# Optimization experiments

Hardware: AMD Instinct MI355X
Metric: run time of the kernel (lower is better)

## Reference

```python
import jax, jax.numpy as jnp
import numpy as np

N = 50000          # nodes
E = 1_600_000      # directed edges (avg degree 32)
C_IN = 512
C_OUT = 64
H1, F1 = 8, 8      # conv1: heads=8, out per head=8
H2 = 1             # conv2: heads_2=1, concat=False
NEG_SLOPE = 0.2    # GATConv default leaky_relu slope
ELU_ALPHA = 0.2    # F.elu(..., alpha=0.2) in forward


def _glorot(key, shape):
    fan_in, fan_out = shape[0], shape[-1]
    lim = jnp.sqrt(6.0 / (fan_in + fan_out))
    return jax.random.uniform(key, shape, jnp.float32, -lim, lim)


def setup_inputs() -> dict:
    key = jax.random.key(0)
    ks = jax.random.split(key, 12)
    x = jax.random.normal(ks[0], (N, C_IN), jnp.float32)
    edge_index = jax.random.randint(ks[1], (2, E), 0, N, jnp.int32)
    # conv1 params
    W1 = _glorot(ks[2], (C_IN, H1 * F1))
    att_src1 = _glorot(ks[3], (H1, F1))
    att_dst1 = _glorot(ks[4], (H1, F1))
    b1 = jnp.zeros((H1 * F1,), jnp.float32)
    # conv2 params (concat=False, heads=1)
    W2 = _glorot(ks[5], (H1 * F1, H2 * C_OUT))
    att_src2 = _glorot(ks[6], (H2, C_OUT))
    att_dst2 = _glorot(ks[7], (H2, C_OUT))
    b2 = jnp.zeros((C_OUT,), jnp.float32)
    return dict(x=x, edge_index=edge_index, W1=W1, att_src1=att_src1,
                att_dst1=att_dst1, b1=b1, W2=W2, att_src2=att_src2,
                att_dst2=att_dst2, b2=b2)


def gat_conv(x, src, dst, W, att_src, att_dst, bias, concat):
    """PyG GATConv (self-loops already appended to src/dst). Eval mode (no dropout)."""
    n = x.shape[0]
    H, F = att_src.shape
    h = (x @ W).reshape(n, H, F)                       # [N,H,F]
    a_src = jnp.sum(h * att_src, axis=-1)              # [N,H]
    a_dst = jnp.sum(h * att_dst, axis=-1)              # [N,H]
    e = jax.nn.leaky_relu(a_src[src] + a_dst[dst], NEG_SLOPE)  # [E',H]
    # segment softmax over incoming edges of each destination node
    m = jax.ops.segment_max(e, dst, num_segments=n)    # [N,H]
    m = jnp.where(jnp.isfinite(m), m, 0.0)
    ex = jnp.exp(e - m[dst])
    denom = jax.ops.segment_sum(ex, dst, num_segments=n)
    alpha = ex / (denom[dst] + 1e-16)                  # [E',H]
    msg = h[src] * alpha[:, :, None]                   # [E',H,F]
    out = jax.ops.segment_sum(msg, dst, num_segments=n)  # [N,H,F]
    out = out.reshape(n, H * F) if concat else out.mean(axis=1)
    return out + bias


def reference(x, edge_index, W1, att_src1, att_dst1, b1,
              W2, att_src2, att_dst2, b2):
    # add self loops once (GATConv default add_self_loops=True)
    loop = jnp.arange(N, dtype=edge_index.dtype)
    src = jnp.concatenate([edge_index[0], loop])
    dst = jnp.concatenate([edge_index[1], loop])
    # dropout layers are identity in eval mode
    h = gat_conv(x, src, dst, W1, att_src1, att_dst1, b1, concat=True)
    h = jax.nn.elu(h, alpha=ELU_ALPHA)
    out = gat_conv(h, src, dst, W2, att_src2, att_dst2, b2, concat=False)
    return out
```

## Files before the change

### kernel.cpp

```cpp
#include <hip/hip_runtime.h>
#include <hip/hip_bf16.h>
#include <hip/hip_fp16.h>

constexpr int NN   = 50000;
constexpr int NE   = 1600000;
constexpr int CIN  = 512;
constexpr int DH   = 64;
constexpr int H1N  = 8;

constexpr int NB     = 98;
constexpr int TILE   = 8192;
constexpr int NTILES = (NE + TILE - 1) / TILE;
constexpr int BCAP   = 20480;

typedef __attribute__((ext_vector_type(8))) short bf16x8v;
typedef __attribute__((ext_vector_type(4))) float f32x4v;

__device__ __forceinline__ float bf(unsigned short u) {
    union { unsigned int i; float f; } v; v.i = ((unsigned int)u) << 16; return v.f;
}
__device__ __forceinline__ float lrelu(float x) { return fmaxf(x, 0.2f * x); }
__device__ __forceinline__ float ldf(const unsigned short* p, size_t i, bool f32) {
    return f32 ? ((const float*)p)[i] : bf(p[i]);
}
__device__ __forceinline__ unsigned short f2bf(float f) {
    union { float f; unsigned int u; } v; v.f = f;
    unsigned int r = (v.u + 0x7fff + ((v.u >> 16) & 1)) >> 16;
    return (unsigned short)r;
}

__global__ __launch_bounds__(256) void gat_detect(const unsigned short* __restrict__ W1,
                                                  int* __restrict__ flag) {
    __shared__ int cnt;
    if (threadIdx.x == 0) cnt = 0;
    __syncthreads();
    int local = 0;
    for (int i = threadIdx.x; i < 4096; i += 256) {
        unsigned short u = W1[i];
        int e = (u >> 7) & 0xFF;
        if (e >= 140) local++;
    }
    atomicAdd(&cnt, local);
    __syncthreads();
    if (threadIdx.x == 0) flag[0] = (cnt > 100) ? 1 : 0;
}


__global__ __launch_bounds__(256) void gat_bucketA(const int* __restrict__ src,
                                                   const int* __restrict__ dst,
                                                   int* __restrict__ gcnt,
                                                   unsigned int* __restrict__ bucketed) {
    __shared__ int hist[NB];
    __shared__ int cur[NB];
    int t = threadIdx.x;
    if (t < NB) hist[t] = 0;
    __syncthreads();
    int base = blockIdx.x * TILE;
    for (int i = t; i < TILE; i += 256) {
        int e = base + i;
        if (e < NE) atomicAdd(&hist[dst[e] >> 9], 1);
    }
    __syncthreads();
    if (t < NB) cur[t] = hist[t] ? atomicAdd(&gcnt[t], hist[t]) : 0;
    __syncthreads();
    for (int i = t; i < TILE; i += 256) {
        int e = base + i;
        if (e < NE) {
            int d = dst[e];
            int b = d >> 9;
            int p = atomicAdd(&cur[b], 1);
            if (p < BCAP)
                bucketed[(size_t)b * BCAP + p] =
                    ((unsigned int)(d & 511) << 16) | (unsigned int)src[e];
        }
    }
}

__global__ __launch_bounds__(128) void gat_bucketscan(const int* __restrict__ gcnt,
                                                      int* __restrict__ boff,
                                                      int* __restrict__ row_ptr) {
    __shared__ int s[128];
    int t = threadIdx.x;
    s[t] = (t < NB) ? gcnt[t] : 0;
    __syncthreads();
    for (int off = 1; off < 128; off <<= 1) {
        int x = s[t];
        int add = (t >= off) ? s[t - off] : 0;
        __syncthreads();
        s[t] = x + add;
        __syncthreads();
    }
    if (t <= NB) boff[t] = (t == 0) ? 0 : s[t - 1];
    if (t == 0) row_ptr[NN] = NE;
}

__global__ __launch_bounds__(256) void gat_bucketB(const unsigned int* __restrict__ bucketed,
                                                   const int* __restrict__ gcnt,
                                                   const int* __restrict__ boff,
                                                   int* __restrict__ row_ptr,
                                                   int* __restrict__ col_idx) {
    __shared__ int hist[512];
    __shared__ int sums[256];
    int t = threadIdx.x;
    int b = blockIdx.x;
    int e0 = boff[b];
    int cnt = gcnt[b]; if (cnt > BCAP) cnt = BCAP;
    const unsigned int* bb = bucketed + (size_t)b * BCAP;
    hist[t] = 0; hist[t + 256] = 0;
    __syncthreads();
    for (int i = t; i < cnt; i += 256)
        atomicAdd(&hist[bb[i] >> 16], 1);
    __syncthreads();
    int a0 = hist[2 * t], a1 = hist[2 * t + 1];
    sums[t] = a0 + a1;
    __syncthreads();
    for (int off = 1; off < 256; off <<= 1) {
        int x = sums[t];
        int add = (t >= off) ? sums[t - off] : 0;
        __syncthreads();
        sums[t] = x + add;
        __syncthreads();
    }
    int excl = (t == 0) ? 0 : sums[t - 1];
    hist[2 * t]     = excl;
    hist[2 * t + 1] = excl + a0;
    int node0 = b << 9;
    if (node0 + 2 * t     < NN) row_ptr[node0 + 2 * t]     = e0 + excl;
    if (node0 + 2 * t + 1 < NN) row_ptr[node0 + 2 * t + 1] = e0 + excl + a0;
    __syncthreads();
    for (int i = t; i < cnt; i += 256) {
        unsigned int pk = bb[i];
        int p = atomicAdd(&hist[pk >> 16], 1);
        col_idx[e0 + p] = (int)(pk & 0xFFFFu);
    }
}


__global__ __launch_bounds__(256) void gat_maxcol(const float* __restrict__ v, int n, int H,
                                                  unsigned int* __restrict__ out) {
    __shared__ float red[256];
    int t = threadIdx.x;
    float mx = -3.4e38f;
    for (int idx = blockIdx.x * 256 + t; idx < n; idx += gridDim.x * 256)
        mx = fmaxf(mx, v[idx]);
    red[t] = mx;
    __syncthreads();
    for (int off = 128; off >= H; off >>= 1) {
        if (t < off) red[t] = fmaxf(red[t], red[t + off]);
        __syncthreads();
    }
    if (t < H) {
        union { float f; unsigned int u; } b; b.f = red[t];
        unsigned int enc = (b.u & 0x80000000u) ? ~b.u : (b.u | 0x80000000u);
        atomicMax(&out[t], enc);
    }
}

__device__ __forceinline__ float gdecode(unsigned int u) {
    union { unsigned int u; float f; } d;
    d.u = (u & 0x80000000u) ? (u ^ 0x80000000u) : ~u;
    return d.f;
}


__global__ __launch_bounds__(256) void gat_transW(const unsigned short* __restrict__ W1,
                                                  const int* __restrict__ flag,
                                                  unsigned short* __restrict__ wts) {
    int idx = blockIdx.x * 256 + threadIdx.x;
    int n = idx >> 9, k = idx & 511;
    if (flag[0] == 0) {
        int o  = n * 1024 + k * 2;
        int os = o ^ ((n & 7) << 4);
        wts[os >> 1] = W1[(size_t)k * DH + n];
    } else {
        float v = ((const float*)W1)[(size_t)k * DH + n];
        unsigned short hi = f2bf(v);
        union { unsigned int u; float f; } hf; hf.u = ((unsigned int)hi) << 16;
        unsigned short lo = f2bf(v - hf.f);
        int q = k >> 7, kk = k & 127;
        int o = q * 32768 + n * 256 + ((kk * 2) ^ ((n & 7) << 4));
        wts[o >> 1]             = hi;
        wts[(o + 16384) >> 1]   = lo;
    }
}


__global__ __launch_bounds__(256) void gat_transW2(const unsigned short* __restrict__ W2,
                                                   const int* __restrict__ flag,
                                                   unsigned short* __restrict__ wts2) {
    int idx = blockIdx.x * 256 + threadIdx.x;
    if (idx >= 4096) return;
    int n = idx & 63, k = idx >> 6;
    unsigned short hi, lo;
    if (flag[0] == 0) {
        hi = W2[(size_t)k * DH + n];
        lo = 0;
    } else {
        float v = ((const float*)W2)[(size_t)k * DH + n];
        hi = f2bf(v);
        union { unsigned int u; float f; } hf; hf.u = ((unsigned int)hi) << 16;
        lo = f2bf(v - hf.f);
    }
    int o = n * 128 + ((k * 2) ^ ((n & 7) << 4));
    wts2[o >> 1]            = hi;
    wts2[(o + 8192) >> 1]   = lo;
}


__global__ __launch_bounds__(256) void gat_gemm1_mfma(const unsigned short* __restrict__ x,
                                                      const unsigned short* __restrict__ wts,
                                                      const unsigned short* __restrict__ as1,
                                                      const unsigned short* __restrict__ ad1,
                                                      const int* __restrict__ flag,
                                                      __half* __restrict__ h1h,
                                                      float* __restrict__ a_s1,
                                                      float* __restrict__ a_d1) {
    if (flag[0] != 0) return;
    __shared__ __align__(16) unsigned short wl[32768];
    int t = threadIdx.x;
#pragma unroll
    for (int it = 0; it < 16; ++it) {
        int c = it * 256 + t;
        *(uint4*)((char*)wl + c * 16) = *(const uint4*)((const char*)wts + c * 16);
    }
    __syncthreads();

    int lane = t & 63, wv = t >> 6;
    int g = lane >> 4;
    int r = lane & 15;
    int chunk = blockIdx.x * 4 + wv;
    if (chunk * 16 >= NN) return;
    int rowbase = chunk * 16;

    int vbase = r * 1024;
    int gx = g * 16;
    int xr = (r & 7) << 4;

    const char* xrow = (const char*)x + ((size_t)(rowbase + r) * CIN + g * 8) * 2;

    f32x4v acc[4];
#pragma unroll
    for (int nt = 0; nt < 4; ++nt) acc[nt] = (f32x4v){0.f, 0.f, 0.f, 0.f};

#pragma unroll 4
    for (int s = 0; s < 16; ++s) {
        union { uint4 u; bf16x8v v; } a;
        a.u = *(const uint4*)(xrow + s * 64);
        int o = vbase + ((s * 64 + gx) ^ xr);
        const char* bp = (const char*)wl + o;
#pragma unroll
        for (int nt = 0; nt < 4; ++nt) {
            union { uint4 u; bf16x8v v; } bv;
            bv.u = *(const uint4*)(bp + nt * 16384);
            acc[nt] = __builtin_amdgcn_mfma_f32_16x16x32_bf16(a.v, bv.v, acc[nt], 0, 0, 0);
        }
    }

    float avs[4], avd[4];
#pragma unroll
    for (int nt = 0; nt < 4; ++nt) {
        avs[nt] = bf(as1[nt * 16 + r]);
        avd[nt] = bf(ad1[nt * 16 + r]);
    }

#pragma unroll
    for (int nt = 0; nt < 4; ++nt) {
#pragma unroll
        for (int i = 0; i < 4; ++i) {
            int row = rowbase + g * 4 + i;
            float v = acc[nt][i];
            h1h[(size_t)row * DH + nt * 16 + r] = __float2half(v);
            float ps = v * avs[nt];
            float pd = v * avd[nt];
            ps += __shfl_xor(ps, 1, 64); ps += __shfl_xor(ps, 2, 64); ps += __shfl_xor(ps, 4, 64);
            pd += __shfl_xor(pd, 1, 64); pd += __shfl_xor(pd, 2, 64); pd += __shfl_xor(pd, 4, 64);
            if ((r & 7) == 0) {
                int head = nt * 2 + (r >> 3);
                a_s1[row * H1N + head] = ps;
                a_d1[row * H1N + head] = pd;
            }
        }
    }
}


__global__ __launch_bounds__(256) void gat_gemm1_mfma_f32(const float* __restrict__ x,
                                                          const unsigned short* __restrict__ wts,
                                                          const float* __restrict__ as1,
                                                          const float* __restrict__ ad1,
                                                          const int* __restrict__ flag,
                                                          __half* __restrict__ h1h,
                                                          float* __restrict__ a_s1,
                                                          float* __restrict__ a_d1) {
    if (flag[0] == 0) return;
    __shared__ __align__(16) unsigned short wl[16384];
    int t = threadIdx.x;
    int lane = t & 63, wv = t >> 6;
    int g = lane >> 4;
    int r = lane & 15;
    int chunk = blockIdx.x * 4 + wv;
    bool active = (chunk * 16 < NN);
    int rowbase = (active ? chunk : 0) * 16;

    int vbase = r * 256;
    int xr = (r & 7) << 4;

    const float* xrow = x + (size_t)(rowbase + r) * CIN + g * 8;

    f32x4v acc[4];
#pragma unroll
    for (int nt = 0; nt < 4; ++nt) acc[nt] = (f32x4v){0.f, 0.f, 0.f, 0.f};

    for (int q = 0; q < 4; ++q) {
        if (q) __syncthreads();
        const uint4* gsrc = (const uint4*)((const char*)wts + q * 32768);
#pragma unroll
        for (int it = 0; it < 8; ++it)
            ((uint4*)wl)[it * 256 + t] = gsrc[it * 256 + t];
        __syncthreads();

#pragma unroll
        for (int s = 0; s < 4; ++s) {
            const float4* xp = (const float4*)(xrow + q * 128 + s * 32);
            float4 v0 = xp[0], v1 = xp[1];
            float xv[8] = {v0.x, v0.y, v0.z, v0.w, v1.x, v1.y, v1.z, v1.w};
            union { unsigned short u[8]; bf16x8v v; } ahi, alo;
#pragma unroll
            for (int i2 = 0; i2 < 8; ++i2) {
                union { float f; unsigned int u; } xb; xb.f = xv[i2];
                unsigned int hb = xb.u & 0xffff0000u;
                union { unsigned int u; float f; } hf; hf.u = hb;
                ahi.u[i2] = (unsigned short)(xb.u >> 16);
                alo.u[i2] = f2bf(xv[i2] - hf.f);
            }
            int o = vbase + ((s * 64 + g * 16) ^ xr);
#pragma unroll
            for (int nt = 0; nt < 4; ++nt) {
                union { uint4 u; bf16x8v v; } bhi, blo;
                bhi.u = *(const uint4*)((const char*)wl + nt * 4096 + o);
                blo.u = *(const uint4*)((const char*)wl + 16384 + nt * 4096 + o);
                acc[nt] = __builtin_amdgcn_mfma_f32_16x16x32_bf16(ahi.v, bhi.v, acc[nt], 0, 0, 0);
                acc[nt] = __builtin_amdgcn_mfma_f32_16x16x32_bf16(ahi.v, blo.v, acc[nt], 0, 0, 0);
                acc[nt] = __builtin_amdgcn_mfma_f32_16x16x32_bf16(alo.v, bhi.v, acc[nt], 0, 0, 0);
            }
        }
    }

    if (!active) return;

    float avs[4], avd[4];
#pragma unroll
    for (int nt = 0; nt < 4; ++nt) {
        avs[nt] = as1[nt * 16 + r];
        avd[nt] = ad1[nt * 16 + r];
    }

#pragma unroll
    for (int nt = 0; nt < 4; ++nt) {
#pragma unroll
        for (int i = 0; i < 4; ++i) {
            int row = rowbase + g * 4 + i;
            float v = acc[nt][i];
            h1h[(size_t)row * DH + nt * 16 + r] = __float2half(v);
            float ps = v * avs[nt];
            float pd = v * avd[nt];
            ps += __shfl_xor(ps, 1, 64); ps += __shfl_xor(ps, 2, 64); ps += __shfl_xor(ps, 4, 64);
            pd += __shfl_xor(pd, 1, 64); pd += __shfl_xor(pd, 2, 64); pd += __shfl_xor(pd, 4, 64);
            if ((r & 7) == 0) {
                int head = nt * 2 + (r >> 3);
                a_s1[row * H1N + head] = ps;
                a_d1[row * H1N + head] = pd;
            }
        }
    }
}


__global__ __launch_bounds__(256) void gat_agg1(const int* __restrict__ row_ptr,
                                                const int* __restrict__ col_idx,
                                                const float* __restrict__ a_s1,
                                                const float* __restrict__ a_d1,
                                                const unsigned int* __restrict__ Gsu,
                                                const __half* __restrict__ h1h,
                                                const unsigned short* __restrict__ b1,
                                                const int* __restrict__ flag,
                                                float* __restrict__ hout) {
    const bool f32 = (flag[0] != 0);
    int i = (blockIdx.x * 256 + threadIdx.x) >> 6;
    int lane = threadIdx.x & 63;
    if (i >= NN) return;
    int ek = lane & 7;
    int eh = lane >> 3;
    int wbase = lane & ~7;

    float adst = a_d1[i * H1N + eh];
    float m = lrelu(gdecode(Gsu[eh]) + adst);

    int jb = row_ptr[i], je = row_ptr[i + 1];
    int deg = je - jb;
    int myidx = (lane < deg) ? col_idx[jb + lane] : 0;

    float wself = __expf(lrelu(a_s1[i * H1N + eh] + adst) - m);
    float denp = (ek == 0) ? wself : 0.f;
    float acc = wself * __half2float(h1h[(size_t)i * DH + lane]);

    for (int j0 = 0; j0 < deg; j0 += 8) {
        int s[8]; int se;
        bool vE = (j0 + ek) < deg;
        if (j0 < 64) {
#pragma unroll
            for (int k = 0; k < 8; ++k) s[k] = __shfl(myidx, j0 + k, 64);
            se = __shfl(myidx, j0 + ek, 64);
        } else {
            int dm1 = deg - 1;
#pragma unroll
            for (int k = 0; k < 8; ++k) {
                int jj = j0 + k; if (jj > dm1) jj = dm1;
                s[k] = col_idx[jb + jj];
            }
            se = col_idx[jb + (vE ? j0 + ek : dm1)];
        }
        float w = __expf(lrelu(a_s1[se * H1N + eh] + adst) - m);
        w = vE ? w : 0.f;
        denp += w;
        float r[8];
#pragma unroll
        for (int k = 0; k < 8; ++k) r[k] = __half2float(h1h[(size_t)s[k] * DH + lane]);
        float ws[8];
#pragma unroll
        for (int k = 0; k < 8; ++k) ws[k] = __shfl(w, wbase + k, 64);
        float a0 = (ws[0] * r[0] + ws[1] * r[1]) + (ws[2] * r[2] + ws[3] * r[3]);
        float a1 = (ws[4] * r[4] + ws[5] * r[5]) + (ws[6] * r[6] + ws[7] * r[7]);
        acc += a0 + a1;
    }
    denp += __shfl_xor(denp, 1, 64);
    denp += __shfl_xor(denp, 2, 64);
    denp += __shfl_xor(denp, 4, 64);

    float val = acc / denp + ldf(b1, lane, f32);
    val = val > 0.f ? val : 0.2f * (__expf(val) - 1.f);
    hout[(size_t)i * DH + lane] = val;
}


__global__ __launch_bounds__(256) void gat_gemm2_mfma(const float* __restrict__ hin,
                                                      const unsigned short* __restrict__ wts2,
                                                      const unsigned short* __restrict__ as2,
                                                      const unsigned short* __restrict__ ad2,
                                                      const int* __restrict__ flag,
                                                      __half* __restrict__ h2h,
                                                      float* __restrict__ a_s2,
                                                      float* __restrict__ a_d2) {
    __shared__ __align__(16) unsigned short wl[8192];
    const bool f32 = (flag[0] != 0);
    int t = threadIdx.x;
#pragma unroll
    for (int it = 0; it < 4; ++it)
        ((uint4*)wl)[it * 256 + t] = ((const uint4*)wts2)[it * 256 + t];
    __syncthreads();

    int lane = t & 63, wv = t >> 6;
    int g = lane >> 4;
    int r = lane & 15;
    int chunk = blockIdx.x * 4 + wv;
    if (chunk * 16 >= NN) return;
    int rowbase = chunk * 16;

    int vbase = r * 128;
    int xr = (r & 7) << 4;

    const float* xrow = hin + (size_t)(rowbase + r) * DH + g * 8;

    f32x4v acc[4];
#pragma unroll
    for (int nt = 0; nt < 4; ++nt) acc[nt] = (f32x4v){0.f, 0.f, 0.f, 0.f};

#pragma unroll
    for (int s = 0; s < 2; ++s) {
        const float4* xp = (const float4*)(xrow + s * 32);
        float4 v0 = xp[0], v1 = xp[1];
        float xv[8] = {v0.x, v0.y, v0.z, v0.w, v1.x, v1.y, v1.z, v1.w};
        union { unsigned short u[8]; bf16x8v v; } ahi, alo;
#pragma unroll
        for (int i2 = 0; i2 < 8; ++i2) {
            union { float f; unsigned int u; } xb; xb.f = xv[i2];
            unsigned int hb = xb.u & 0xffff0000u;
            union { unsigned int u; float f; } hf; hf.u = hb;
            ahi.u[i2] = (unsigned short)(xb.u >> 16);
            alo.u[i2] = f2bf(xv[i2] - hf.f);
        }
        int o = vbase + ((s * 64 + g * 16) ^ xr);
#pragma unroll
        for (int nt = 0; nt < 4; ++nt) {
            union { uint4 u; bf16x8v v; } bhi, blo;
            bhi.u = *(const uint4*)((const char*)wl + nt * 2048 + o);
            blo.u = *(const uint4*)((const char*)wl + 8192 + nt * 2048 + o);
            acc[nt] = __builtin_amdgcn_mfma_f32_16x16x32_bf16(ahi.v, bhi.v, acc[nt], 0, 0, 0);
            acc[nt] = __builtin_amdgcn_mfma_f32_16x16x32_bf16(ahi.v, blo.v, acc[nt], 0, 0, 0);
            acc[nt] = __builtin_amdgcn_mfma_f32_16x16x32_bf16(alo.v, bhi.v, acc[nt], 0, 0, 0);
        }
    }

    float avs[4], avd[4];
#pragma unroll
    for (int nt = 0; nt < 4; ++nt) {
        avs[nt] = ldf(as2, nt * 16 + r, f32);
        avd[nt] = ldf(ad2, nt * 16 + r, f32);
    }

#pragma unroll
    for (int i = 0; i < 4; ++i) {
        int row = rowbase + g * 4 + i;
        float ps = 0.f, pd = 0.f;
#pragma unroll
        for (int nt = 0; nt < 4; ++nt) {
            float v = acc[nt][i];
            h2h[(size_t)row * DH + nt * 16 + r] = __float2half(v);
            ps += v * avs[nt];
            pd += v * avd[nt];
        }
        ps += __shfl_xor(ps, 1, 64); ps += __shfl_xor(ps, 2, 64);
        ps += __shfl_xor(ps, 4, 64); ps += __shfl_xor(ps, 8, 64);
        pd += __shfl_xor(pd, 1, 64); pd += __shfl_xor(pd, 2, 64);
        pd += __shfl_xor(pd, 4, 64); pd += __shfl_xor(pd, 8, 64);
        if (r == 0) { a_s2[row] = ps; a_d2[row] = pd; }
    }
}


__global__ __launch_bounds__(256) void gat_agg2(const int* __restrict__ row_ptr,
                                                const int* __restrict__ col_idx,
                                                const float* __restrict__ a_s2,
                                                const float* __restrict__ a_d2,
                                                const unsigned int* __restrict__ Gsu2,
                                                const __half* __restrict__ h2h,
                                                const unsigned short* __restrict__ b2,
                                                const int* __restrict__ flag,
                                                void* __restrict__ out) {
    const bool f32 = (flag[0] != 0);
    int i = (blockIdx.x * 256 + threadIdx.x) >> 6;
    int lane = threadIdx.x & 63;
    if (i >= NN) return;
    int ek = lane & 7;

    float adst = a_d2[i];
    float m = lrelu(gdecode(Gsu2[0]) + adst);

    int jb = row_ptr[i], je = row_ptr[i + 1];
    int deg = je - jb;
    int myidx = (lane < deg) ? col_idx[jb + lane] : 0;

    float wself = __expf(lrelu(a_s2[i] + adst) - m);
    float denp = (ek == 0) ? wself : 0.f;
    float acc = wself * __half2float(h2h[(size_t)i * DH + lane]);

    for (int j0 = 0; j0 < deg; j0 += 8) {
        int s[8]; int se;
        bool vE = (j0 + ek) < deg;
        if (j0 < 64) {
#pragma unroll
            for (int k = 0; k < 8; ++k) s[k] = __shfl(myidx, j0 + k, 64);
            se = __shfl(myidx, j0 + ek, 64);
        } else {
            int dm1 = deg - 1;
#pragma unroll
            for (int k = 0; k < 8; ++k) {
                int jj = j0 + k; if (jj > dm1) jj = dm1;
                s[k] = col_idx[jb + jj];
            }
            se = col_idx[jb + (vE ? j0 + ek : dm1)];
        }
        float w = __expf(lrelu(a_s2[se] + adst) - m);
        w = vE ? w : 0.f;
        denp += w;
        float r[8];
#pragma unroll
        for (int k = 0; k < 8; ++k) r[k] = __half2float(h2h[(size_t)s[k] * DH + lane]);
        float ws[8];
#pragma unroll
        for (int k = 0; k < 8; ++k) ws[k] = __shfl(w, k, 64);
        float a0 = (ws[0] * r[0] + ws[1] * r[1]) + (ws[2] * r[2] + ws[3] * r[3]);
        float a1 = (ws[4] * r[4] + ws[5] * r[5]) + (ws[6] * r[6] + ws[7] * r[7]);
        acc += a0 + a1;
    }
    denp += __shfl_xor(denp, 1, 64);
    denp += __shfl_xor(denp, 2, 64);
    denp += __shfl_xor(denp, 4, 64);

    float val = acc / denp + ldf(b2, lane, f32);
    size_t oi = (size_t)i * DH + lane;
    if (f32) ((float*)out)[oi] = val;
    else     ((__hip_bfloat16*)out)[oi] = __float2bfloat16(val);
}


static void* g_scratch = nullptr;

extern "C" void kernel_launch(void* const* d_in, const int* in_sizes, int n_in,
                              void* d_out, int out_size, void* d_ws, size_t ws_size,
                              hipStream_t stream) {
    const unsigned short* x   = (const unsigned short*)d_in[0];
    const int*            ei  = (const int*)d_in[1];
    const unsigned short* W1  = (const unsigned short*)d_in[2];
    const unsigned short* as1 = (const unsigned short*)d_in[3];
    const unsigned short* ad1 = (const unsigned short*)d_in[4];
    const unsigned short* b1  = (const unsigned short*)d_in[5];
    const unsigned short* W2  = (const unsigned short*)d_in[6];
    const unsigned short* as2 = (const unsigned short*)d_in[7];
    const unsigned short* ad2 = (const unsigned short*)d_in[8];
    const unsigned short* b2  = (const unsigned short*)d_in[9];

    const int* srcv = ei;
    const int* dstv = ei + NE;

    const size_t off_wts   = 64;
    const size_t off_wts2  = off_wts + 131072;
    const size_t off_h1h   = off_wts2 + 16384;
    const size_t off_hmid  = off_h1h + (size_t)NN * DH * 2;
    const size_t off_as1   = off_hmid + (size_t)NN * DH * 4;
    const size_t off_ad1   = off_as1 + (size_t)NN * H1N * 4;
    const size_t off_rp    = off_ad1 + (size_t)NN * H1N * 4;
    const size_t off_ci    = off_rp + (size_t)(NN + 1) * 4;
    const size_t off_bk    = off_ci + (size_t)NE * 4;
    const size_t off_gcnt  = off_bk + (size_t)NB * BCAP * 4;
    const size_t off_gsu   = off_gcnt + 128 * 4;
    const size_t off_boff  = off_gsu + 16 * 4;
    const size_t need      = off_boff + 128 * 4;

    void* wsbase = d_ws;
    if (ws_size < need) {
        if (g_scratch == nullptr) hipMalloc(&g_scratch, need);
        wsbase = g_scratch;
    }
    char* B = (char*)wsbase;

    int*            flag = (int*)B;
    unsigned short* wts  = (unsigned short*)(B + off_wts);
    unsigned short* wts2 = (unsigned short*)(B + off_wts2);
    __half*         h1h  = (__half*)(B + off_h1h);
    float*          hmid = (float*)(B + off_hmid);
    float*          a_s1 = (float*)(B + off_as1);
    float*          a_d1 = (float*)(B + off_ad1);
    int*         row_ptr = (int*)(B + off_rp);
    int*         col_idx = (int*)(B + off_ci);
    unsigned int* bucketed = (unsigned int*)(B + off_bk);
    int*            gcnt = (int*)(B + off_gcnt);
    unsigned int*   Gsu  = (unsigned int*)(B + off_gsu);
    int*            boff = (int*)(B + off_boff);
    __half* h2h  = h1h;
    float* a_s2 = a_s1;
    float* a_d2 = a_d1;

    hipMemsetAsync(gcnt, 0, (128 + 16) * sizeof(int), stream);
    gat_detect<<<1, 256, 0, stream>>>(W1, flag);

    gat_bucketA   <<<NTILES, 256, 0, stream>>>(srcv, dstv, gcnt, bucketed);
    gat_bucketscan<<<1, 128, 0, stream>>>(gcnt, boff, row_ptr);
    gat_bucketB   <<<NB, 256, 0, stream>>>(bucketed, gcnt, boff, row_ptr, col_idx);

    gat_transW <<<128, 256, 0, stream>>>(W1, flag, wts);
    gat_transW2<<<16, 256, 0, stream>>>(W2, flag, wts2);
    int gemmb = (3125 + 3) / 4;
    gat_gemm1_mfma    <<<gemmb, 256, 0, stream>>>(x, wts, as1, ad1, flag, h1h, a_s1, a_d1);
    gat_gemm1_mfma_f32<<<gemmb, 256, 0, stream>>>((const float*)x, wts,
                                                  (const float*)as1, (const float*)ad1,
                                                  flag, h1h, a_s1, a_d1);

    gat_maxcol<<<64, 256, 0, stream>>>(a_s1, NN * H1N, 8, Gsu);

    int nb = (NN * 64 + 255) / 256;
    gat_agg1<<<nb, 256, 0, stream>>>(row_ptr, col_idx, a_s1, a_d1, Gsu, h1h, b1, flag, hmid);

    gat_gemm2_mfma<<<gemmb, 256, 0, stream>>>(hmid, wts2, as2, ad2, flag, h2h, a_s2, a_d2);

    gat_maxcol<<<32, 256, 0, stream>>>(a_s2, NN, 1, Gsu + 8);

    gat_agg2<<<nb, 256, 0, stream>>>(row_ptr, col_idx, a_s2, a_d2, Gsu + 8, h2h, b2, flag, d_out);
}
```

Measured before the change: 414.0 us.

## Sub-sort CSR neighbors by source-range tile and aggregate tile by tile

The CSR build now groups each destination node's edges into four source-index ranges and stores four row pointers per node. Both aggregation kernels walk the ranges in order, so concurrent waves tend to gather from nearby regions of the feature table, which is meant to improve cache locality. In exchange, each range is processed in its own batches of 8, which adds partially filled batches and loop overhead. The bucket histogram and row-pointer storage also grow fourfold.

```diff
diff --git a/kernel.cpp b/kernel.cpp
--- a/kernel.cpp
+++ b/kernel.cpp
@@ -27,6 +27,9 @@
     union { float f; unsigned int u; } v; v.f = f;
     unsigned int r = (v.u + 0x7fff + ((v.u >> 16) & 1)) >> 16;
     return (unsigned short)r;
+}
+__device__ __forceinline__ int srctile(int s) {
+    return (s >= 12500) + (s >= 25000) + (s >= 37500);
 }
 
 __global__ __launch_bounds__(256) void gat_detect(const unsigned short* __restrict__ W1,
@@ -78,7 +81,7 @@
 
 __global__ __launch_bounds__(128) void gat_bucketscan(const int* __restrict__ gcnt,
                                                       int* __restrict__ boff,
-                                                      int* __restrict__ row_ptr) {
+                                                      int* __restrict__ rp2) {
     __shared__ int s[128];
     int t = threadIdx.x;
     s[t] = (t < NB) ? gcnt[t] : 0;
@@ -91,28 +94,34 @@
         __syncthreads();
     }
     if (t <= NB) boff[t] = (t == 0) ? 0 : s[t - 1];
-    if (t == 0) row_ptr[NN] = NE;
-}
+    if (t == 0) rp2[NN * 4] = NE;
+}
+
 
 __global__ __launch_bounds__(256) void gat_bucketB(const unsigned int* __restrict__ bucketed,
                                                    const int* __restrict__ gcnt,
                                                    const int* __restrict__ boff,
-                                                   int* __restrict__ row_ptr,
+                                                   int* __restrict__ rp2,
                                                    int* __restrict__ col_idx) {
-    __shared__ int hist[512];
+    __shared__ int hist[2048];
     __shared__ int sums[256];
     int t = threadIdx.x;
     int b = blockIdx.x;
     int e0 = boff[b];
     int cnt = gcnt[b]; if (cnt > BCAP) cnt = BCAP;
     const unsigned int* bb = bucketed + (size_t)b * BCAP;
-    hist[t] = 0; hist[t + 256] = 0;
-    __syncthreads();
-    for (int i = t; i < cnt; i += 256)
-        atomicAdd(&hist[bb[i] >> 16], 1);
-    __syncthreads();
-    int a0 = hist[2 * t], a1 = hist[2 * t + 1];
-    sums[t] = a0 + a1;
+    for (int z = t; z < 2048; z += 256) hist[z] = 0;
+    __syncthreads();
+    for (int i = t; i < cnt; i += 256) {
+        unsigned int pk = bb[i];
+        int sv = (int)(pk & 0xFFFFu);
+        atomicAdd(&hist[((pk >> 16) << 2) | srctile(sv)], 1);
+    }
+    __syncthreads();
+    int loc[8]; int s = 0;
+#pragma unroll
+    for (int u = 0; u < 8; ++u) { loc[u] = hist[t * 8 + u]; s += loc[u]; }
+    sums[t] = s;
     __syncthreads();
     for (int off = 1; off < 256; off <<= 1) {
         int x = sums[t];
@@ -121,17 +130,21 @@
         sums[t] = x + add;
         __syncthreads();
     }
-    int excl = (t == 0) ? 0 : sums[t - 1];
-    hist[2 * t]     = excl;
-    hist[2 * t + 1] = excl + a0;
+    int run = (t == 0) ? 0 : sums[t - 1];
     int node0 = b << 9;
-    if (node0 + 2 * t     < NN) row_ptr[node0 + 2 * t]     = e0 + excl;
-    if (node0 + 2 * t + 1 < NN) row_ptr[node0 + 2 * t + 1] = e0 + excl + a0;
+#pragma unroll
+    for (int u = 0; u < 8; ++u) {
+        hist[t * 8 + u] = run;
+        int node = node0 + 2 * t + (u >> 2);
+        if (node < NN) rp2[node * 4 + (u & 3)] = e0 + run;
+        run += loc[u];
+    }
     __syncthreads();
     for (int i = t; i < cnt; i += 256) {
         unsigned int pk = bb[i];
-        int p = atomicAdd(&hist[pk >> 16], 1);
-        col_idx[e0 + p] = (int)(pk & 0xFFFFu);
+        int sv = (int)(pk & 0xFFFFu);
+        int p = atomicAdd(&hist[((pk >> 16) << 2) | srctile(sv)], 1);
+        col_idx[e0 + p] = sv;
     }
 }
 
@@ -376,7 +389,7 @@
 }
 
 
-__global__ __launch_bounds__(256) void gat_agg1(const int* __restrict__ row_ptr,
+__global__ __launch_bounds__(256) void gat_agg1(const int* __restrict__ rp2,
                                                 const int* __restrict__ col_idx,
                                                 const float* __restrict__ a_s1,
                                                 const float* __restrict__ a_d1,
@@ -396,42 +409,48 @@
     float adst = a_d1[i * H1N + eh];
     float m = lrelu(gdecode(Gsu[eh]) + adst);
 
-    int jb = row_ptr[i], je = row_ptr[i + 1];
-    int deg = je - jb;
+    int jb = rp2[i * 4];
+    int deg = rp2[i * 4 + 4] - jb;
     int myidx = (lane < deg) ? col_idx[jb + lane] : 0;
 
     float wself = __expf(lrelu(a_s1[i * H1N + eh] + adst) - m);
     float denp = (ek == 0) ? wself : 0.f;
     float acc = wself * __half2float(h1h[(size_t)i * DH + lane]);
 
-    for (int j0 = 0; j0 < deg; j0 += 8) {
-        int s[8]; int se;
-        bool vE = (j0 + ek) < deg;
-        if (j0 < 64) {
-#pragma unroll
-            for (int k = 0; k < 8; ++k) s[k] = __shfl(myidx, j0 + k, 64);
-            se = __shfl(myidx, j0 + ek, 64);
-        } else {
-            int dm1 = deg - 1;
-#pragma unroll
-            for (int k = 0; k < 8; ++k) {
-                int jj = j0 + k; if (jj > dm1) jj = dm1;
-                s[k] = col_idx[jb + jj];
+#pragma unroll
+    for (int tl = 0; tl < 4; ++tl) {
+        int js  = rp2[i * 4 + tl] - jb;
+        int jeR = rp2[i * 4 + tl + 1] - jb;
+        for (int j0 = js; j0 < jeR; j0 += 8) {
+            bool vE = (j0 + ek) < jeR;
+            int s[8]; int se;
+            if (j0 + 8 <= 64) {
+#pragma unroll
+                for (int k = 0; k < 8; ++k) s[k] = __shfl(myidx, j0 + k, 64);
+                se = __shfl(myidx, j0 + ek, 64);
+            } else {
+                int last = jeR - 1;
+#pragma unroll
+                for (int k = 0; k < 8; ++k) {
+                    int jj = j0 + k; if (jj > last) jj = last;
+                    s[k] = (jj < 64) ? __shfl(myidx, jj, 64) : col_idx[jb + jj];
+                }
+                int jje = vE ? (j0 + ek) : last;
+                se = (jje < 64) ? __shfl(myidx, jje, 64) : col_idx[jb + jje];
             }
-            se = col_idx[jb + (vE ? j0 + ek : dm1)];
-        }
-        float w = __expf(lrelu(a_s1[se * H1N + eh] + adst) - m);
-        w = vE ? w : 0.f;
-        denp += w;
-        float r[8];
-#pragma unroll
-        for (int k = 0; k < 8; ++k) r[k] = __half2float(h1h[(size_t)s[k] * DH + lane]);
-        float ws[8];
-#pragma unroll
-        for (int k = 0; k < 8; ++k) ws[k] = __shfl(w, wbase + k, 64);
-        float a0 = (ws[0] * r[0] + ws[1] * r[1]) + (ws[2] * r[2] + ws[3] * r[3]);
-        float a1 = (ws[4] * r[4] + ws[5] * r[5]) + (ws[6] * r[6] + ws[7] * r[7]);
-        acc += a0 + a1;
+            float w = __expf(lrelu(a_s1[se * H1N + eh] + adst) - m);
+            w = vE ? w : 0.f;
+            denp += w;
+            float r[8];
+#pragma unroll
+            for (int k = 0; k < 8; ++k) r[k] = __half2float(h1h[(size_t)s[k] * DH + lane]);
+            float ws[8];
+#pragma unroll
+            for (int k = 0; k < 8; ++k) ws[k] = __shfl(w, wbase + k, 64);
+            float a0 = (ws[0] * r[0] + ws[1] * r[1]) + (ws[2] * r[2] + ws[3] * r[3]);
+            float a1 = (ws[4] * r[4] + ws[5] * r[5]) + (ws[6] * r[6] + ws[7] * r[7]);
+            acc += a0 + a1;
+        }
     }
     denp += __shfl_xor(denp, 1, 64);
     denp += __shfl_xor(denp, 2, 64);
@@ -528,7 +547,7 @@
 }
 
 
-__global__ __launch_bounds__(256) void gat_agg2(const int* __restrict__ row_ptr,
+__global__ __launch_bounds__(256) void gat_agg2(const int* __restrict__ rp2,
                                                 const int* __restrict__ col_idx,
                                                 const float* __restrict__ a_s2,
                                                 const float* __restrict__ a_d2,
@@ -546,42 +565,48 @@
     float adst = a_d2[i];
     float m = lrelu(gdecode(Gsu2[0]) + adst);
 
-    int jb = row_ptr[i], je = row_ptr[i + 1];
-    int deg = je - jb;
+    int jb = rp2[i * 4];
+    int deg = rp2[i * 4 + 4] - jb;
     int myidx = (lane < deg) ? col_idx[jb + lane] : 0;
 
     float wself = __expf(lrelu(a_s2[i] + adst) - m);
     float denp = (ek == 0) ? wself : 0.f;
     float acc = wself * __half2float(h2h[(size_t)i * DH + lane]);
 
-    for (int j0 = 0; j0 < deg; j0 += 8) {
-        int s[8]; int se;
-        bool vE = (j0 + ek) < deg;
-        if (j0 < 64) {
-#pragma unroll
-            for (int k = 0; k < 8; ++k) s[k] = __shfl(myidx, j0 + k, 64);
-            se = __shfl(myidx, j0 + ek, 64);
-        } else {
-            int dm1 = deg - 1;
-#pragma unroll
-            for (int k = 0; k < 8; ++k) {
-                int jj = j0 + k; if (jj > dm1) jj = dm1;
-                s[k] = col_idx[jb + jj];
+#pragma unroll
+    for (int tl = 0; tl < 4; ++tl) {
+        int js  = rp2[i * 4 + tl] - jb;
+        int jeR = rp2[i * 4 + tl + 1] - jb;
+        for (int j0 = js; j0 < jeR; j0 += 8) {
+            bool vE = (j0 + ek) < jeR;
+            int s[8]; int se;
+            if (j0 + 8 <= 64) {
+#pragma unroll
+                for (int k = 0; k < 8; ++k) s[k] = __shfl(myidx, j0 + k, 64);
+                se = __shfl(myidx, j0 + ek, 64);
+            } else {
+                int last = jeR - 1;
+#pragma unroll
+                for (int k = 0; k < 8; ++k) {
+                    int jj = j0 + k; if (jj > last) jj = last;
+                    s[k] = (jj < 64) ? __shfl(myidx, jj, 64) : col_idx[jb + jj];
+                }
+                int jje = vE ? (j0 + ek) : last;
+                se = (jje < 64) ? __shfl(myidx, jje, 64) : col_idx[jb + jje];
             }
-            se = col_idx[jb + (vE ? j0 + ek : dm1)];
-        }
-        float w = __expf(lrelu(a_s2[se] + adst) - m);
-        w = vE ? w : 0.f;
-        denp += w;
-        float r[8];
-#pragma unroll
-        for (int k = 0; k < 8; ++k) r[k] = __half2float(h2h[(size_t)s[k] * DH + lane]);
-        float ws[8];
-#pragma unroll
-        for (int k = 0; k < 8; ++k) ws[k] = __shfl(w, k, 64);
-        float a0 = (ws[0] * r[0] + ws[1] * r[1]) + (ws[2] * r[2] + ws[3] * r[3]);
-        float a1 = (ws[4] * r[4] + ws[5] * r[5]) + (ws[6] * r[6] + ws[7] * r[7]);
-        acc += a0 + a1;
+            float w = __expf(lrelu(a_s2[se] + adst) - m);
+            w = vE ? w : 0.f;
+            denp += w;
+            float r[8];
+#pragma unroll
+            for (int k = 0; k < 8; ++k) r[k] = __half2float(h2h[(size_t)s[k] * DH + lane]);
+            float ws[8];
+#pragma unroll
+            for (int k = 0; k < 8; ++k) ws[k] = __shfl(w, k, 64);
+            float a0 = (ws[0] * r[0] + ws[1] * r[1]) + (ws[2] * r[2] + ws[3] * r[3]);
+            float a1 = (ws[4] * r[4] + ws[5] * r[5]) + (ws[6] * r[6] + ws[7] * r[7]);
+            acc += a0 + a1;
+        }
     }
     denp += __shfl_xor(denp, 1, 64);
     denp += __shfl_xor(denp, 2, 64);
@@ -619,8 +644,8 @@
     const size_t off_hmid  = off_h1h + (size_t)NN * DH * 2;
     const size_t off_as1   = off_hmid + (size_t)NN * DH * 4;
     const size_t off_ad1   = off_as1 + (size_t)NN * H1N * 4;
-    const size_t off_rp    = off_ad1 + (size_t)NN * H1N * 4;
-    const size_t off_ci    = off_rp + (size_t)(NN + 1) * 4;
+    const size_t off_rp2   = off_ad1 + (size_t)NN * H1N * 4;
+    const size_t off_ci    = off_rp2 + ((size_t)NN * 4 + 4) * 4;
     const size_t off_bk    = off_ci + (size_t)NE * 4;
     const size_t off_gcnt  = off_bk + (size_t)NB * BCAP * 4;
     const size_t off_gsu   = off_gcnt + 128 * 4;
@@ -641,7 +666,7 @@
     float*          hmid = (float*)(B + off_hmid);
     float*          a_s1 = (float*)(B + off_as1);
     float*          a_d1 = (float*)(B + off_ad1);
-    int*         row_ptr = (int*)(B + off_rp);
+    int*            rp2  = (int*)(B + off_rp2);
     int*         col_idx = (int*)(B + off_ci);
     unsigned int* bucketed = (unsigned int*)(B + off_bk);
     int*            gcnt = (int*)(B + off_gcnt);
@@ -655,8 +680,8 @@
     gat_detect<<<1, 256, 0, stream>>>(W1, flag);
 
     gat_bucketA   <<<NTILES, 256, 0, stream>>>(srcv, dstv, gcnt, bucketed);
-    gat_bucketscan<<<1, 128, 0, stream>>>(gcnt, boff, row_ptr);
-    gat_bucketB   <<<NB, 256, 0, stream>>>(bucketed, gcnt, boff, row_ptr, col_idx);
+    gat_bucketscan<<<1, 128, 0, stream>>>(gcnt, boff, rp2);
+    gat_bucketB   <<<NB, 256, 0, stream>>>(bucketed, gcnt, boff, rp2, col_idx);
 
     gat_transW <<<128, 256, 0, stream>>>(W1, flag, wts);
     gat_transW2<<<16, 256, 0, stream>>>(W2, flag, wts2);
@@ -669,11 +694,11 @@
     gat_maxcol<<<64, 256, 0, stream>>>(a_s1, NN * H1N, 8, Gsu);
 
     int nb = (NN * 64 + 255) / 256;
-    gat_agg1<<<nb, 256, 0, stream>>>(row_ptr, col_idx, a_s1, a_d1, Gsu, h1h, b1, flag, hmid);
+    gat_agg1<<<nb, 256, 0, stream>>>(rp2, col_idx, a_s1, a_d1, Gsu, h1h, b1, flag, hmid);
 
     gat_gemm2_mfma<<<gemmb, 256, 0, stream>>>(hmid, wts2, as2, ad2, flag, h2h, a_s2, a_d2);
 
     gat_maxcol<<<32, 256, 0, stream>>>(a_s2, NN, 1, Gsu + 8);
 
-    gat_agg2<<<nb, 256, 0, stream>>>(row_ptr, col_idx, a_s2, a_d2, Gsu + 8, h2h, b2, flag, d_out);
-}
+    gat_agg2<<<nb, 256, 0, stream>>>(rp2, col_idx, a_s2, a_d2, Gsu + 8, h2h, b2, flag, d_out);
+}
```

New measurement: 444.0 us. 7.3% more time.
